# Kernel optimization log

Hardware: AMD Instinct MI355X
Metric: run time of the kernel (lower is better)

The kernel has to match this reference:

```python
import jax, jax.numpy as jnp
import numpy as np

B, S, D = 1, 2048, 2048
H, KVH = 32, 8
HD = D // H          # 64
N_REP = H // KVH     # 4
ROPE_THETA = 10000.0
NEG = -1e9


def setup_inputs() -> dict:
    key = jax.random.key(0)
    ks = jax.random.split(key, 8)
    x = jax.random.normal(ks[0], (B, S, D), dtype=jnp.float32)
    # RoPE tables: freqs_cis[t, j] = exp(i * t * theta^{-2j/HD}), j in [0, HD/2)
    inv_freq = 1.0 / (ROPE_THETA ** (jnp.arange(0, HD, 2, dtype=jnp.float32) / HD))
    angles = jnp.arange(S, dtype=jnp.float32)[:, None] * inv_freq[None, :]  # (S, HD/2)
    freqs_cos = jnp.cos(angles)
    freqs_sin = jnp.sin(angles)
    # causal additive mask (S, S)
    mask = jnp.where(jnp.tril(jnp.ones((S, S), dtype=bool)), 0.0, NEG).astype(jnp.float32)
    sc = 0.02
    wq = jax.random.normal(ks[1], (D, H * HD), dtype=jnp.float32) * sc
    wk = jax.random.normal(ks[2], (D, KVH * HD), dtype=jnp.float32) * sc
    wv = jax.random.normal(ks[3], (D, KVH * HD), dtype=jnp.float32) * sc
    wo = jax.random.normal(ks[4], (H * HD, D), dtype=jnp.float32) * sc
    fw = jax.random.normal(ks[5], (HD, HD), dtype=jnp.float32) * sc
    fb = jnp.zeros((HD,), dtype=jnp.float32)
    return {"x": x, "freqs_cos": freqs_cos, "freqs_sin": freqs_sin, "mask": mask,
            "wq": wq, "wk": wk, "wv": wv, "wo": wo, "fw": fw, "fb": fb,
            "start_pos": 0}


def _rope(t, cos, sin):
    # t: (B, S, h, HD) -> complex rotate pairs along last dim
    tr = t.reshape(*t.shape[:-1], HD // 2, 2)
    c = cos[None, :, None, :]  # (1, S, 1, HD/2)
    s = sin[None, :, None, :]
    re = tr[..., 0] * c - tr[..., 1] * s
    im = tr[..., 0] * s + tr[..., 1] * c
    return jnp.stack([re, im], axis=-1).reshape(t.shape)


def reference(x, freqs_cos, freqs_sin, mask, wq, wk, wv, wo, fw, fb, start_pos):
    b, s, _ = x.shape
    xq = (x @ wq).reshape(b, s, H, HD)
    xk = (x @ wk).reshape(b, s, KVH, HD)
    xv = (x @ wv).reshape(b, s, KVH, HD)
    xq = _rope(xq, freqs_cos, freqs_sin)
    xk = _rope(xk, freqs_cos, freqs_sin)
    # GQA: repeat kv heads (repeat_interleave on head dim)
    keys = jnp.repeat(xk, N_REP, axis=2)    # (b, s, H, HD)
    values = jnp.repeat(xv, N_REP, axis=2)
    q = xq.transpose(0, 2, 1, 3)            # (b, H, s, HD)
    k = keys.transpose(0, 2, 1, 3)
    v = values.transpose(0, 2, 1, 3)
    scores = jnp.einsum("bhqd,bhkd->bhqk", q, k) / np.sqrt(HD).astype(np.float32)
    scores = scores + mask[None, None, :, :]
    probs = jax.nn.softmax(scores.astype(jnp.float32), axis=-1).astype(q.dtype)
    out = jnp.einsum("bhqk,bhkd->bhqd", probs, v)  # (b, H, s, HD)
    # shared per-head FFN: Linear(HD, HD) + SiLU, vectorized over heads
    out = jax.nn.silu(out @ fw + fb)
    out = out.transpose(0, 2, 1, 3).reshape(b, s, H * HD)
    return out @ wo
```

## Files before the change

kernel.cpp:

```cpp
#include <hip/hip_runtime.h>
#include <stdint.h>

#define S_LEN 2048
#define DMODEL 2048
#define NH 32
#define NKV 8
#define HD 64

typedef __attribute__((ext_vector_type(8))) __bf16 bf16x8;
typedef __attribute__((ext_vector_type(4))) float f32x4;
typedef __attribute__((ext_vector_type(16))) float f32x16;

__device__ __forceinline__ unsigned short f2bf(float f) {
    union { float f; uint32_t u; } v; v.f = f;
    uint32_t u = v.u;
    u += 0x7FFFu + ((u >> 16) & 1u);
    return (unsigned short)(u >> 16);
}

__device__ __forceinline__ uint32_t cvt_pk_bf16(float lo, float hi) {
    uint32_t r;
    asm("v_cvt_pk_bf16_f32 %0, %1, %2" : "=v"(r) : "v"(lo), "v"(hi));
    return r;
}

#define GLDS16(g, l)                                                          \
    __builtin_amdgcn_global_load_lds(                                         \
        (const __attribute__((address_space(1))) unsigned int*)(g),           \
        (__attribute__((address_space(3))) unsigned int*)(l), 16, 0, 0)

__device__ const int kUQT[24] = {15,15,7,14,14,13,13,6,12,12,11,11,5,10,10,9,9,4,8,8,3,2,1,0};
__device__ const int kUCH[24] = {0,1,0,0,1,0,1,0,0,1,0,1,0,0,1,0,1,0,0,1,0,0,0,0};
__device__ const int kUSP[24] = {1,1,0,1,1,1,1,0,1,1,1,1,0,1,1,1,1,0,1,1,0,0,0,0};

__global__ void cast_bf16_kernel(const float* __restrict__ src,
                                 unsigned short* __restrict__ dst, int n) {
    int g = (blockIdx.x * blockDim.x + threadIdx.x) * 8;
    if (g >= n) return;
    float4 a = *(const float4*)&src[g];
    float4 b = *(const float4*)&src[g + 4];
    unsigned short o[8];
    o[0] = f2bf(a.x); o[1] = f2bf(a.y); o[2] = f2bf(a.z); o[3] = f2bf(a.w);
    o[4] = f2bf(b.x); o[5] = f2bf(b.y); o[6] = f2bf(b.z); o[7] = f2bf(b.w);
    *(uint4*)&dst[g] = *(const uint4*)o;
}

__global__ void prep_transpose_kernel(
    const float* __restrict__ wq, const float* __restrict__ wk,
    const float* __restrict__ wv, const float* __restrict__ wo,
    const float* __restrict__ fw, unsigned short* __restrict__ wqkvT,
    unsigned short* __restrict__ woT, unsigned short* __restrict__ fwT) {
    __shared__ float tile[32][33];
    const int z = blockIdx.z;
    const float* src;
    unsigned short* dst;
    int R, C;
    if (z == 0)      { src = wq; dst = wqkvT;                         R = 2048; C = 2048; }
    else if (z == 1) { src = wk; dst = wqkvT + (size_t)2048 * 2048;   R = 2048; C = 512;  if (blockIdx.x >= 16) return; }
    else if (z == 2) { src = wv; dst = wqkvT + (size_t)2560 * 2048;   R = 2048; C = 512;  if (blockIdx.x >= 16) return; }
    else if (z == 3) { src = wo; dst = woT;                           R = 2048; C = 2048; }
    else             { src = fw; dst = fwT;                           R = 64;   C = 64;   if (blockIdx.x >= 2 || blockIdx.y >= 2) return; }
    int c0 = blockIdx.x * 32, r0 = blockIdx.y * 32;
    int tx = threadIdx.x, ty = threadIdx.y;
#pragma unroll
    for (int i = 0; i < 32; i += 8)
        tile[ty + i][tx] = src[(size_t)(r0 + ty + i) * C + c0 + tx];
    __syncthreads();
#pragma unroll
    for (int i = 0; i < 32; i += 8)
        dst[(size_t)(c0 + ty + i) * R + r0 + tx] = f2bf(tile[tx][ty + i]);
}

template <int MODE>
__global__ __launch_bounds__(256) void gemm_bt_kernel(
    const unsigned short* __restrict__ A, const unsigned short* __restrict__ BT,
    float* __restrict__ C0, unsigned short* __restrict__ Qb,
    unsigned short* __restrict__ Kb, unsigned short* __restrict__ VT,
    const float* __restrict__ fcos, const float* __restrict__ fsin,
    int M, int N, int K) {
    __shared__ unsigned short As[3][128 * 32];
    __shared__ unsigned short Bs[3][64 * 32];
    const int t = threadIdx.x;
    const int lane = t & 63, wave = t >> 6;
    const int wr = wave >> 1, wc = wave & 1;
    const int gx = gridDim.x;
    const int nwg = gx * gridDim.y;
    const int wg = blockIdx.y * gx + blockIdx.x;
    const int swz = (wg & 7) * (nwg >> 3) + (wg >> 3);
    const int m0 = (swz % gx) * 128, n0 = (swz / gx) * 64;
    const int l15 = lane & 15, lhi = lane >> 4;
    f32x4 acc[4][2] = {};
    const unsigned short* ga = A + (size_t)(m0 + (t >> 2)) * K + (t & 3) * 8;
    const unsigned short* gb = BT + (size_t)(n0 + (t >> 2)) * K + (t & 3) * 8;
    const int nk = K >> 5;

#define GSTAGE(buf, kt)                                                       \
    {                                                                         \
        const int k0_ = (kt) * 32;                                            \
        GLDS16(ga + k0_, &As[buf][t * 8]);                                    \
        GLDS16(ga + (size_t)64 * K + k0_, &As[buf][t * 8 + 64 * 32]);         \
        if (t < 256) GLDS16(gb + k0_, &Bs[buf][t * 8]);                       \
    }

    GSTAGE(0, 0);
    GSTAGE(1, 1);

    int cb = 0, pfb = 2;
#pragma unroll 1
    for (int kt = 0; kt < nk; ++kt) {
        if (kt + 1 < nk) asm volatile("s_waitcnt vmcnt(3)" ::: "memory");
        else             asm volatile("s_waitcnt vmcnt(0)" ::: "memory");
        __builtin_amdgcn_s_barrier();
        __builtin_amdgcn_sched_barrier(0);
        if (kt + 2 < nk) GSTAGE(pfb, kt + 2);
        pfb = (pfb == 2) ? 0 : pfb + 1;
        const int mycb = cb;
        cb = (cb == 2) ? 0 : cb + 1;
        bf16x8 af[4], bfr[2];
#pragma unroll
        for (int m = 0; m < 4; m++)
            af[m] = *(const bf16x8*)&As[mycb][(wr * 64 + m * 16 + l15) * 32 + lhi * 8];
#pragma unroll
        for (int n = 0; n < 2; n++)
            bfr[n] = *(const bf16x8*)&Bs[mycb][(wc * 32 + n * 16 + l15) * 32 + lhi * 8];
#pragma unroll
        for (int m = 0; m < 4; m++)
#pragma unroll
            for (int n = 0; n < 2; n++)
                acc[m][n] = __builtin_amdgcn_mfma_f32_16x16x32_bf16(
                    af[m], bfr[n], acc[m][n], 0, 0, 0);
    }
#undef GSTAGE
    if (MODE == 0) {
#pragma unroll
        for (int m = 0; m < 4; m++) {
            int row = m0 + wr * 64 + m * 16 + lhi * 4;
#pragma unroll
            for (int n = 0; n < 2; n++) {
                int col = n0 + wc * 32 + n * 16 + l15;
#pragma unroll
                for (int r = 0; r < 4; r++)
                    C0[(size_t)(row + r) * N + col] = acc[m][n][r];
            }
        }
    } else {
        const int nblk = n0 >> 6;
        if (nblk < 40) {
            const float CS = 0.125f * 1.44269504f;
            const bool isQ = (nblk < 32);
            unsigned short* dst = isQ ? Qb + (size_t)nblk * (S_LEN * HD)
                                      : Kb + (size_t)(nblk - 32) * (S_LEN * HD);
#pragma unroll
            for (int m = 0; m < 4; m++) {
#pragma unroll
                for (int n = 0; n < 2; n++) {
                    int col = wc * 32 + n * 16 + l15;
                    int i = col >> 1;
                    float sgn = (col & 1) ? 1.f : -1.f;
#pragma unroll
                    for (int r = 0; r < 4; r++) {
                        int s = m0 + wr * 64 + m * 16 + lhi * 4 + r;
                        float c = fcos[s * 32 + i], sn = fsin[s * 32 + i];
                        float v = acc[m][n][r];
                        float pv = __shfl_xor(v, 1);
                        float o = fmaf(pv, sgn * sn, v * c);
                        if (isQ) o *= CS;
                        dst[(size_t)s * HD + col] = f2bf(o);
                    }
                }
            }
        } else {
            const int kvh = nblk - 40;
            unsigned short* ldsT = (unsigned short*)As;
            __syncthreads();
#pragma unroll
            for (int m = 0; m < 4; m++)
#pragma unroll
                for (int n = 0; n < 2; n++) {
                    int d = wc * 32 + n * 16 + l15;
#pragma unroll
                    for (int r = 0; r < 4; r++) {
                        int sl = wr * 64 + m * 16 + lhi * 4 + r;
                        ldsT[d * 130 + sl] = f2bf(acc[m][n][r]);
                    }
                }
            __syncthreads();
            const int d = t >> 2, sc = (t & 3) * 32;
            unsigned short* dst = VT + ((size_t)kvh * HD + d) * S_LEN + m0 + sc;
            const unsigned short* srcl = &ldsT[d * 130 + sc];
#pragma unroll
            for (int j = 0; j < 16; j++)
                ((uint32_t*)dst)[j] = *(const uint32_t*)&srcl[2 * j];
        }
    }
}

__global__ __launch_bounds__(256) void flash_kernel(
    const unsigned short* __restrict__ Q, const unsigned short* __restrict__ Kg,
    const unsigned short* __restrict__ VTg, unsigned short* __restrict__ O,
    float* __restrict__ Opart, float* __restrict__ ML) {
    __shared__ unsigned short Ks[3][4096];
    __shared__ unsigned short Vs[3][4096];
    const int t = threadIdx.x, lane = t & 63, wave = t >> 6;
    const int l31 = lane & 31, hi = lane >> 5;
    const int bid = blockIdx.x;
    const int h = bid & 31, u = bid >> 5;
    const int qt = kUQT[u], ch = kUCH[u], sp = kUSP[u];
    const int kvh = h >> 2;

    const int kt0 = sp ? ch * (qt + 1) : 0;
    const int ktN = sp ? kt0 + qt + 1 : 2 * qt + 2;

    const int srow = t >> 3;
    const int scol = ((t & 7) * 8) ^ ((srow & 7) * 8);
    const unsigned short* gk = Kg + ((size_t)kvh * S_LEN + srow) * HD + scol;
    const unsigned short* gv = VTg + ((size_t)kvh * HD + srow) * S_LEN + scol;

    const int q0 = qt * 128;
    const int qw0 = q0 + wave * 32;
    const int q = qw0 + l31;

    const unsigned short* qp = Q + ((size_t)h * S_LEN + q) * HD + hi * 8;
    bf16x8 qf0 = *(const bf16x8*)(qp);
    bf16x8 qf1 = *(const bf16x8*)(qp + 16);
    bf16x8 qf2 = *(const bf16x8*)(qp + 32);
    bf16x8 qf3 = *(const bf16x8*)(qp + 48);

    f32x16 oacc0 = {}, oacc1 = {};
    float mrun = -1e30f, lrun = 0.f;

    {
        const size_t kva = (size_t)kt0 * 64, kvb = kva + 64;
        GLDS16(gk + kva * HD, &Ks[0][t * 8]);
        GLDS16(gk + (kva + 32) * HD, &Ks[0][t * 8 + 2048]);
        GLDS16(gv + kva, &Vs[0][t * 8]);
        GLDS16(gv + (size_t)32 * S_LEN + kva, &Vs[0][t * 8 + 2048]);
        GLDS16(gk + kvb * HD, &Ks[1][t * 8]);
        GLDS16(gk + (kvb + 32) * HD, &Ks[1][t * 8 + 2048]);
        GLDS16(gv + kvb, &Vs[1][t * 8]);
        GLDS16(gv + (size_t)32 * S_LEN + kvb, &Vs[1][t * 8 + 2048]);
    }

    int cb = 0, pfb = 2;
#pragma unroll 1
    for (int kt = kt0; kt < ktN; ++kt) {
        if (kt + 1 < ktN) asm volatile("s_waitcnt vmcnt(4)" ::: "memory");
        else              asm volatile("s_waitcnt vmcnt(0)" ::: "memory");
        __builtin_amdgcn_s_barrier();
        __builtin_amdgcn_sched_barrier(0);
        if (kt + 2 < ktN) {
            const size_t kvp = (size_t)(kt + 2) * 64;
            GLDS16(gk + kvp * HD, &Ks[pfb][t * 8]);
            GLDS16(gk + (kvp + 32) * HD, &Ks[pfb][t * 8 + 2048]);
            GLDS16(gv + kvp, &Vs[pfb][t * 8]);
            GLDS16(gv + (size_t)32 * S_LEN + kvp, &Vs[pfb][t * 8 + 2048]);
        }
        pfb = (pfb == 2) ? 0 : pfb + 1;
        const int kv0 = kt * 64;
        const int mycb = cb;
        cb = (cb == 2) ? 0 : cb + 1;
        if (kv0 > qw0 + 31) continue;
        const unsigned short* ksb = Ks[mycb];
        const unsigned short* vsb = Vs[mycb];
        const int sw = (l31 & 7) * 8;
        f32x16 s0 = {}, s1 = {};
#pragma unroll
        for (int kc = 0; kc < 4; kc++) {
            bf16x8 k0 = *(const bf16x8*)&ksb[l31 * 64 + ((16 * kc + 8 * hi) ^ sw)];
            bf16x8 k1 = *(const bf16x8*)&ksb[(32 + l31) * 64 + ((16 * kc + 8 * hi) ^ sw)];
            bf16x8 qc = (kc == 0) ? qf0 : (kc == 1) ? qf1 : (kc == 2) ? qf2 : qf3;
            s0 = __builtin_amdgcn_mfma_f32_32x32x16_bf16(k0, qc, s0, 0, 0, 0);
            s1 = __builtin_amdgcn_mfma_f32_32x32x16_bf16(k1, qc, s1, 0, 0, 0);
        }
        float p0[16], p1[16];
        if (kv0 + 63 <= qw0) {
#pragma unroll
            for (int r = 0; r < 16; r++) { p0[r] = s0[r]; p1[r] = s1[r]; }
        } else {
#pragma unroll
            for (int r = 0; r < 16; r++) {
                int rr = (r & 3) + 8 * (r >> 2) + 4 * hi;
                p0[r] = (kv0 + rr <= q) ? s0[r] : -1e30f;
                p1[r] = (kv0 + 32 + rr <= q) ? s1[r] : -1e30f;
            }
        }
        float t8[8];
#pragma unroll
        for (int r = 0; r < 8; r++)
            t8[r] = fmaxf(fmaxf(p0[r], p0[r + 8]), fmaxf(p1[r], p1[r + 8]));
        float lm = fmaxf(fmaxf(fmaxf(t8[0], t8[4]), fmaxf(t8[1], t8[5])),
                         fmaxf(fmaxf(t8[2], t8[6]), fmaxf(t8[3], t8[7])));
        if (!__all(lm - mrun <= 8.f)) {
            float rm = fmaxf(lm, __shfl_xor(lm, 32));
            float mnew = fmaxf(mrun, rm);
            float sc = exp2f(mrun - mnew);
            mrun = mnew;
            lrun *= sc;
            oacc0 *= sc;
            oacc1 *= sc;
        }
#pragma unroll
        for (int r = 0; r < 16; r++) {
            p0[r] = exp2f(p0[r] - mrun);
            p1[r] = exp2f(p1[r] - mrun);
        }
        float sA = 0.f, sB = 0.f, sC = 0.f, sD = 0.f;
#pragma unroll
        for (int r = 0; r < 4; r++) {
            sA += p0[r] + p1[r];
            sB += p0[r + 4] + p1[r + 4];
            sC += p0[r + 8] + p1[r + 8];
            sD += p0[r + 12] + p1[r + 12];
        }
        lrun += (sA + sB) + (sC + sD);
        bf16x8 pf[4];
#pragma unroll
        for (int kc = 0; kc < 4; kc++) {
            const int sub = (kc & 1) * 8;
            uint32_t Wl0, Wl1, Wh0, Wh1;
            if (kc < 2) {
                Wl0 = cvt_pk_bf16(p0[sub + 0], p0[sub + 1]);
                Wl1 = cvt_pk_bf16(p0[sub + 2], p0[sub + 3]);
                Wh0 = cvt_pk_bf16(p0[sub + 4], p0[sub + 5]);
                Wh1 = cvt_pk_bf16(p0[sub + 6], p0[sub + 7]);
            } else {
                Wl0 = cvt_pk_bf16(p1[sub + 0], p1[sub + 1]);
                Wl1 = cvt_pk_bf16(p1[sub + 2], p1[sub + 3]);
                Wh0 = cvt_pk_bf16(p1[sub + 4], p1[sub + 5]);
                Wh1 = cvt_pk_bf16(p1[sub + 6], p1[sub + 7]);
            }
            uint32_t sw0 = hi ? Wl0 : Wh0, sw1 = hi ? Wl1 : Wh1;
            uint32_t rc0 = __shfl_xor((int)sw0, 32);
            uint32_t rc1 = __shfl_xor((int)sw1, 32);
            uint32_t kp0 = hi ? Wh0 : Wl0, kp1 = hi ? Wh1 : Wl1;
            uint32_t F0 = hi ? rc0 : kp0;
            uint32_t F1 = hi ? rc1 : kp1;
            uint32_t F2 = hi ? kp0 : rc0;
            uint32_t F3 = hi ? kp1 : rc1;
            uint4 fu = {F0, F1, F2, F3};
            pf[kc] = *(const bf16x8*)&fu;
        }
#pragma unroll
        for (int kc = 0; kc < 4; kc++) {
            bf16x8 v0 = *(const bf16x8*)&vsb[l31 * 64 + ((16 * kc + 8 * hi) ^ sw)];
            bf16x8 v1 = *(const bf16x8*)&vsb[(32 + l31) * 64 + ((16 * kc + 8 * hi) ^ sw)];
            oacc0 = __builtin_amdgcn_mfma_f32_32x32x16_bf16(v0, pf[kc], oacc0, 0, 0, 0);
            oacc1 = __builtin_amdgcn_mfma_f32_32x32x16_bf16(v1, pf[kc], oacc1, 0, 0, 0);
        }
    }
    lrun += __shfl_xor(lrun, 32);
    const int qrow = wave * 32 + l31;
    if (sp) {
        const int pidx = (h * 8 + (qt - 8)) * 2 + ch;
        float* po = Opart + ((size_t)pidx * 128 + qrow) * 64 + 4 * hi;
#pragma unroll
        for (int g = 0; g < 4; g++) {
            float4 a = {oacc0[4 * g], oacc0[4 * g + 1], oacc0[4 * g + 2], oacc0[4 * g + 3]};
            *(float4*)(po + 8 * g) = a;
            float4 b = {oacc1[4 * g], oacc1[4 * g + 1], oacc1[4 * g + 2], oacc1[4 * g + 3]};
            *(float4*)(po + 32 + 8 * g) = b;
        }
        if (hi == 0) {
            ML[((size_t)pidx * 128 + qrow) * 2] = mrun;
            ML[((size_t)pidx * 128 + qrow) * 2 + 1] = lrun;
        }
    } else {
        float rinv = 1.f / lrun;
        unsigned short* ob = O + ((size_t)h * S_LEN + q) * HD + 4 * hi;
#pragma unroll
        for (int g = 0; g < 4; g++) {
            uint32_t a0 = cvt_pk_bf16(oacc0[4 * g] * rinv, oacc0[4 * g + 1] * rinv);
            uint32_t a1 = cvt_pk_bf16(oacc0[4 * g + 2] * rinv, oacc0[4 * g + 3] * rinv);
            uint2 u0 = {a0, a1};
            *(uint2*)(ob + 8 * g) = u0;
            uint32_t b0 = cvt_pk_bf16(oacc1[4 * g] * rinv, oacc1[4 * g + 1] * rinv);
            uint32_t b1 = cvt_pk_bf16(oacc1[4 * g + 2] * rinv, oacc1[4 * g + 3] * rinv);
            uint2 u1 = {b0, b1};
            *(uint2*)(ob + 32 + 8 * g) = u1;
        }
    }
}

__global__ __launch_bounds__(256) void flash_combine_kernel(
    const float* __restrict__ Opart, const float* __restrict__ ML,
    unsigned short* __restrict__ attn) {
    const int bid = blockIdx.x;
    const int h = bid & 31, j = bid >> 5;
    const int qt = 8 + j;
    const int t = threadIdx.x;
    const int qrow = t >> 1, d0 = (t & 1) * 32;
    const int base = (h * 8 + j) * 2;
    const float mA = ML[((size_t)base * 128 + qrow) * 2];
    const float lA = ML[((size_t)base * 128 + qrow) * 2 + 1];
    const float mB = ML[((size_t)(base + 1) * 128 + qrow) * 2];
    const float lB = ML[((size_t)(base + 1) * 128 + qrow) * 2 + 1];
    const float m = fmaxf(mA, mB);
    const float wA = exp2f(mA - m), wB = exp2f(mB - m);
    const float rinv = 1.f / (lA * wA + lB * wB);
    const float* pA = Opart + ((size_t)base * 128 + qrow) * 64 + d0;
    const float* pB = Opart + ((size_t)(base + 1) * 128 + qrow) * 64 + d0;
    unsigned short* po = attn + ((size_t)h * S_LEN + qt * 128 + qrow) * HD + d0;
#pragma unroll
    for (int dd = 0; dd < 32; dd += 8) {
        float4 a0 = *(const float4*)&pA[dd], a1 = *(const float4*)&pA[dd + 4];
        float4 b0 = *(const float4*)&pB[dd], b1 = *(const float4*)&pB[dd + 4];
        unsigned short o[8];
        o[0] = f2bf((a0.x * wA + b0.x * wB) * rinv);
        o[1] = f2bf((a0.y * wA + b0.y * wB) * rinv);
        o[2] = f2bf((a0.z * wA + b0.z * wB) * rinv);
        o[3] = f2bf((a0.w * wA + b0.w * wB) * rinv);
        o[4] = f2bf((a1.x * wA + b1.x * wB) * rinv);
        o[5] = f2bf((a1.y * wA + b1.y * wB) * rinv);
        o[6] = f2bf((a1.z * wA + b1.z * wB) * rinv);
        o[7] = f2bf((a1.w * wA + b1.w * wB) * rinv);
        *(uint4*)&po[dd] = *(const uint4*)o;
    }
}

__global__ __launch_bounds__(256) void fw_silu_kernel(
    const unsigned short* __restrict__ AT, const unsigned short* __restrict__ fwT,
    const float* __restrict__ fb, unsigned short* __restrict__ h2) {
    const int t = threadIdx.x, lane = t & 63, wave = t >> 6;
    const int l15 = lane & 15, lhi = lane >> 4;
    const int r0 = blockIdx.x * 64 + wave * 16;
    const unsigned short* ap = AT + (size_t)(r0 + l15) * HD + lhi * 8;
    bf16x8 a0 = *(const bf16x8*)ap;
    bf16x8 a1 = *(const bf16x8*)(ap + 32);
    f32x4 acc[4] = {};
#pragma unroll
    for (int nb = 0; nb < 4; nb++) {
        const unsigned short* bp = fwT + (size_t)(nb * 16 + l15) * HD + lhi * 8;
        bf16x8 b0 = *(const bf16x8*)bp;
        bf16x8 b1 = *(const bf16x8*)(bp + 32);
        acc[nb] = __builtin_amdgcn_mfma_f32_16x16x32_bf16(a0, b0, acc[nb], 0, 0, 0);
        acc[nb] = __builtin_amdgcn_mfma_f32_16x16x32_bf16(a1, b1, acc[nb], 0, 0, 0);
    }
#pragma unroll
    for (int nb = 0; nb < 4; nb++) {
        int col = nb * 16 + l15;
        float bias = fb[col];
#pragma unroll
        for (int r = 0; r < 4; r++) {
            int row = r0 + lhi * 4 + r;
            int s = row & (S_LEN - 1), hh = row >> 11;
            float x = acc[nb][r] + bias;
            float sg = 1.f / (1.f + exp2f(-x * 1.44269504f));
            h2[(size_t)s * DMODEL + hh * HD + col] = f2bf(x * sg);
        }
    }
}

extern "C" void kernel_launch(void* const* d_in, const int* in_sizes, int n_in,
                              void* d_out, int out_size, void* d_ws, size_t ws_size,
                              hipStream_t stream) {
    const float* x = (const float*)d_in[0];
    const float* fcos = (const float*)d_in[1];
    const float* fsin = (const float*)d_in[2];
    const float* wq = (const float*)d_in[4];
    const float* wk = (const float*)d_in[5];
    const float* wv = (const float*)d_in[6];
    const float* wo = (const float*)d_in[7];
    const float* fw = (const float*)d_in[8];
    const float* fb = (const float*)d_in[9];
    float* out = (float*)d_out;

    char* ws = (char*)d_ws;
    size_t off = 0;
    auto alloc = [&](size_t bytes) {
        void* p = ws + off;
        off += (bytes + 255) & ~(size_t)255;
        return p;
    };
    unsigned short* wqkvT = (unsigned short*)alloc((size_t)3072 * 2048 * 2);
    unsigned short* woT   = (unsigned short*)alloc((size_t)2048 * 2048 * 2);
    unsigned short* fwT   = (unsigned short*)alloc((size_t)64 * 64 * 2);
    unsigned short* Qb    = (unsigned short*)alloc((size_t)NH * S_LEN * HD * 2);
    unsigned short* Kb    = (unsigned short*)alloc((size_t)NKV * S_LEN * HD * 2);
    unsigned short* VT    = (unsigned short*)alloc((size_t)NKV * HD * S_LEN * 2);
    unsigned short* xb    = (unsigned short*)alloc((size_t)2048 * 2048 * 2);
    float*          ML    = (float*)alloc((size_t)512 * 128 * 2 * 4);
    unsigned short* attn  = (unsigned short*)alloc((size_t)NH * S_LEN * HD * 2);
    float*          Opart = (float*)alloc((size_t)512 * 128 * 64 * 4);
    unsigned short* h2 = xb;

    cast_bf16_kernel<<<2048, 256, 0, stream>>>(x, xb, 2048 * 2048);
    prep_transpose_kernel<<<dim3(64, 64, 5), dim3(32, 8), 0, stream>>>(
        wq, wk, wv, wo, fw, wqkvT, woT, fwT);

    gemm_bt_kernel<1><<<dim3(16, 48), 256, 0, stream>>>(
        xb, wqkvT, nullptr, Qb, Kb, VT, fcos, fsin, 2048, 3072, 2048);

    flash_kernel<<<768, 256, 0, stream>>>(Qb, Kb, VT, attn, Opart, ML);
    flash_combine_kernel<<<256, 256, 0, stream>>>(Opart, ML, attn);

    fw_silu_kernel<<<1024, 256, 0, stream>>>(attn, fwT, fb, h2);

    gemm_bt_kernel<0><<<dim3(16, 32), 256, 0, stream>>>(
        h2, woT, out, nullptr, nullptr, nullptr, nullptr, nullptr,
        2048, 2048, 2048);
}
```

Baseline: 169.7 us.

## Halve flash KV tile to 32 and fuse x cast into prep kernel

The flash attention kernel now streams K/V in 32-row tiles instead of 64. It uses half the LDS per stage, one QK MFMA chain per tile and a new V swizzle, and doubles the iteration count. The causal range bounds and split boundaries are recomputed accordingly. Separately, the fp32-to-bf16 cast of x is merged into the weight transpose prep kernel as an extra grid z-slice, saving one launch. Smaller tiles cut LDS use and register pressure, possibly raising occupancy and giving finer causal skipping, at the cost of more barriers and loop overhead per unit of work.

```diff
diff --git a/kernel.cpp b/kernel.cpp
--- a/kernel.cpp
+++ b/kernel.cpp
@@ -33,35 +33,32 @@
 __device__ const int kUCH[24] = {0,1,0,0,1,0,1,0,0,1,0,1,0,0,1,0,1,0,0,1,0,0,0,0};
 __device__ const int kUSP[24] = {1,1,0,1,1,1,1,0,1,1,1,1,0,1,1,1,1,0,1,1,0,0,0,0};
 
-__global__ void cast_bf16_kernel(const float* __restrict__ src,
-                                 unsigned short* __restrict__ dst, int n) {
-    int g = (blockIdx.x * blockDim.x + threadIdx.x) * 8;
-    if (g >= n) return;
-    float4 a = *(const float4*)&src[g];
-    float4 b = *(const float4*)&src[g + 4];
-    unsigned short o[8];
-    o[0] = f2bf(a.x); o[1] = f2bf(a.y); o[2] = f2bf(a.z); o[3] = f2bf(a.w);
-    o[4] = f2bf(b.x); o[5] = f2bf(b.y); o[6] = f2bf(b.z); o[7] = f2bf(b.w);
-    *(uint4*)&dst[g] = *(const uint4*)o;
-}
-
-__global__ void prep_transpose_kernel(
+__global__ void prep_kernel(
     const float* __restrict__ wq, const float* __restrict__ wk,
     const float* __restrict__ wv, const float* __restrict__ wo,
-    const float* __restrict__ fw, unsigned short* __restrict__ wqkvT,
-    unsigned short* __restrict__ woT, unsigned short* __restrict__ fwT) {
+    const float* __restrict__ fw, const float* __restrict__ x,
+    unsigned short* __restrict__ wqkvT, unsigned short* __restrict__ woT,
+    unsigned short* __restrict__ fwT, unsigned short* __restrict__ xb) {
+    const int z = blockIdx.z;
+    const int tx = threadIdx.x, ty = threadIdx.y;
+    if (z == 5) {
+        int base = (blockIdx.y * 64 + blockIdx.x) * 1024 + (ty * 32 + tx) * 4;
+        float4 a = *(const float4*)&x[base];
+        ushort4 o;
+        o.x = f2bf(a.x); o.y = f2bf(a.y); o.z = f2bf(a.z); o.w = f2bf(a.w);
+        *(ushort4*)&xb[base] = o;
+        return;
+    }
     __shared__ float tile[32][33];
-    const int z = blockIdx.z;
     const float* src;
     unsigned short* dst;
     int R, C;
-    if (z == 0)      { src = wq; dst = wqkvT;                         R = 2048; C = 2048; }
-    else if (z == 1) { src = wk; dst = wqkvT + (size_t)2048 * 2048;   R = 2048; C = 512;  if (blockIdx.x >= 16) return; }
-    else if (z == 2) { src = wv; dst = wqkvT + (size_t)2560 * 2048;   R = 2048; C = 512;  if (blockIdx.x >= 16) return; }
-    else if (z == 3) { src = wo; dst = woT;                           R = 2048; C = 2048; }
-    else             { src = fw; dst = fwT;                           R = 64;   C = 64;   if (blockIdx.x >= 2 || blockIdx.y >= 2) return; }
+    if (z == 0)      { src = wq; dst = wqkvT;                       R = 2048; C = 2048; }
+    else if (z == 1) { src = wk; dst = wqkvT + (size_t)2048 * 2048; R = 2048; C = 512;  if (blockIdx.x >= 16) return; }
+    else if (z == 2) { src = wv; dst = wqkvT + (size_t)2560 * 2048; R = 2048; C = 512;  if (blockIdx.x >= 16) return; }
+    else if (z == 3) { src = wo; dst = woT;                         R = 2048; C = 2048; }
+    else             { src = fw; dst = fwT;                         R = 64;   C = 64;   if (blockIdx.x >= 2 || blockIdx.y >= 2) return; }
     int c0 = blockIdx.x * 32, r0 = blockIdx.y * 32;
-    int tx = threadIdx.x, ty = threadIdx.y;
 #pragma unroll
     for (int i = 0; i < 32; i += 8)
         tile[ty + i][tx] = src[(size_t)(r0 + ty + i) * C + c0 + tx];
@@ -199,8 +196,8 @@
     const unsigned short* __restrict__ Q, const unsigned short* __restrict__ Kg,
     const unsigned short* __restrict__ VTg, unsigned short* __restrict__ O,
     float* __restrict__ Opart, float* __restrict__ ML) {
-    __shared__ unsigned short Ks[3][4096];
-    __shared__ unsigned short Vs[3][4096];
+    __shared__ unsigned short Ks[3][2048];
+    __shared__ unsigned short Vs[3][2048];
     const int t = threadIdx.x, lane = t & 63, wave = t >> 6;
     const int l31 = lane & 31, hi = lane >> 5;
     const int bid = blockIdx.x;
@@ -208,13 +205,15 @@
     const int qt = kUQT[u], ch = kUCH[u], sp = kUSP[u];
     const int kvh = h >> 2;
 
-    const int kt0 = sp ? ch * (qt + 1) : 0;
-    const int ktN = sp ? kt0 + qt + 1 : 2 * qt + 2;
+    const int kt0 = sp ? ch * (2 * qt + 2) : 0;
+    const int ktN = kt0 + (sp ? (2 * qt + 2) : (4 * qt + 4));
 
     const int srow = t >> 3;
     const int scol = ((t & 7) * 8) ^ ((srow & 7) * 8);
     const unsigned short* gk = Kg + ((size_t)kvh * S_LEN + srow) * HD + scol;
-    const unsigned short* gv = VTg + ((size_t)kvh * HD + srow) * S_LEN + scol;
+    const int vrow = t >> 2;
+    const int vcol = (((t & 3) ^ (vrow & 3)) * 8);
+    const unsigned short* gv = VTg + ((size_t)kvh * HD + vrow) * S_LEN + vcol;
 
     const int q0 = qt * 128;
     const int qw0 = q0 + wave * 32;
@@ -229,65 +228,53 @@
     f32x16 oacc0 = {}, oacc1 = {};
     float mrun = -1e30f, lrun = 0.f;
 
-    {
-        const size_t kva = (size_t)kt0 * 64, kvb = kva + 64;
-        GLDS16(gk + kva * HD, &Ks[0][t * 8]);
-        GLDS16(gk + (kva + 32) * HD, &Ks[0][t * 8 + 2048]);
-        GLDS16(gv + kva, &Vs[0][t * 8]);
-        GLDS16(gv + (size_t)32 * S_LEN + kva, &Vs[0][t * 8 + 2048]);
-        GLDS16(gk + kvb * HD, &Ks[1][t * 8]);
-        GLDS16(gk + (kvb + 32) * HD, &Ks[1][t * 8 + 2048]);
-        GLDS16(gv + kvb, &Vs[1][t * 8]);
-        GLDS16(gv + (size_t)32 * S_LEN + kvb, &Vs[1][t * 8 + 2048]);
-    }
+#define FSTAGE(buf, kt)                                                       \
+    {                                                                         \
+        const size_t kv_ = (size_t)(kt) * 32;                                 \
+        GLDS16(gk + kv_ * HD, &Ks[buf][t * 8]);                               \
+        GLDS16(gv + kv_, &Vs[buf][t * 8]);                                    \
+    }
+
+    FSTAGE(0, kt0);
+    FSTAGE(1, kt0 + 1);
 
     int cb = 0, pfb = 2;
 #pragma unroll 1
     for (int kt = kt0; kt < ktN; ++kt) {
-        if (kt + 1 < ktN) asm volatile("s_waitcnt vmcnt(4)" ::: "memory");
+        if (kt + 1 < ktN) asm volatile("s_waitcnt vmcnt(2)" ::: "memory");
         else              asm volatile("s_waitcnt vmcnt(0)" ::: "memory");
         __builtin_amdgcn_s_barrier();
         __builtin_amdgcn_sched_barrier(0);
-        if (kt + 2 < ktN) {
-            const size_t kvp = (size_t)(kt + 2) * 64;
-            GLDS16(gk + kvp * HD, &Ks[pfb][t * 8]);
-            GLDS16(gk + (kvp + 32) * HD, &Ks[pfb][t * 8 + 2048]);
-            GLDS16(gv + kvp, &Vs[pfb][t * 8]);
-            GLDS16(gv + (size_t)32 * S_LEN + kvp, &Vs[pfb][t * 8 + 2048]);
-        }
+        if (kt + 2 < ktN) FSTAGE(pfb, kt + 2);
         pfb = (pfb == 2) ? 0 : pfb + 1;
-        const int kv0 = kt * 64;
+        const int kv0 = kt * 32;
         const int mycb = cb;
         cb = (cb == 2) ? 0 : cb + 1;
         if (kv0 > qw0 + 31) continue;
         const unsigned short* ksb = Ks[mycb];
         const unsigned short* vsb = Vs[mycb];
         const int sw = (l31 & 7) * 8;
-        f32x16 s0 = {}, s1 = {};
+        f32x16 s0 = {};
 #pragma unroll
         for (int kc = 0; kc < 4; kc++) {
             bf16x8 k0 = *(const bf16x8*)&ksb[l31 * 64 + ((16 * kc + 8 * hi) ^ sw)];
-            bf16x8 k1 = *(const bf16x8*)&ksb[(32 + l31) * 64 + ((16 * kc + 8 * hi) ^ sw)];
             bf16x8 qc = (kc == 0) ? qf0 : (kc == 1) ? qf1 : (kc == 2) ? qf2 : qf3;
             s0 = __builtin_amdgcn_mfma_f32_32x32x16_bf16(k0, qc, s0, 0, 0, 0);
-            s1 = __builtin_amdgcn_mfma_f32_32x32x16_bf16(k1, qc, s1, 0, 0, 0);
-        }
-        float p0[16], p1[16];
-        if (kv0 + 63 <= qw0) {
-#pragma unroll
-            for (int r = 0; r < 16; r++) { p0[r] = s0[r]; p1[r] = s1[r]; }
+        }
+        float p0[16];
+        if (kv0 + 31 <= qw0) {
+#pragma unroll
+            for (int r = 0; r < 16; r++) p0[r] = s0[r];
         } else {
 #pragma unroll
             for (int r = 0; r < 16; r++) {
                 int rr = (r & 3) + 8 * (r >> 2) + 4 * hi;
                 p0[r] = (kv0 + rr <= q) ? s0[r] : -1e30f;
-                p1[r] = (kv0 + 32 + rr <= q) ? s1[r] : -1e30f;
             }
         }
         float t8[8];
 #pragma unroll
-        for (int r = 0; r < 8; r++)
-            t8[r] = fmaxf(fmaxf(p0[r], p0[r + 8]), fmaxf(p1[r], p1[r + 8]));
+        for (int r = 0; r < 8; r++) t8[r] = fmaxf(p0[r], p0[r + 8]);
         float lm = fmaxf(fmaxf(fmaxf(t8[0], t8[4]), fmaxf(t8[1], t8[5])),
                          fmaxf(fmaxf(t8[2], t8[6]), fmaxf(t8[3], t8[7])));
         if (!__all(lm - mrun <= 8.f)) {
@@ -300,35 +287,22 @@
             oacc1 *= sc;
         }
 #pragma unroll
-        for (int r = 0; r < 16; r++) {
-            p0[r] = exp2f(p0[r] - mrun);
-            p1[r] = exp2f(p1[r] - mrun);
-        }
-        float sA = 0.f, sB = 0.f, sC = 0.f, sD = 0.f;
+        for (int r = 0; r < 16; r++) p0[r] = exp2f(p0[r] - mrun);
+        float sA = 0.f, sB = 0.f;
 #pragma unroll
         for (int r = 0; r < 4; r++) {
-            sA += p0[r] + p1[r];
-            sB += p0[r + 4] + p1[r + 4];
-            sC += p0[r + 8] + p1[r + 8];
-            sD += p0[r + 12] + p1[r + 12];
-        }
-        lrun += (sA + sB) + (sC + sD);
-        bf16x8 pf[4];
-#pragma unroll
-        for (int kc = 0; kc < 4; kc++) {
-            const int sub = (kc & 1) * 8;
-            uint32_t Wl0, Wl1, Wh0, Wh1;
-            if (kc < 2) {
-                Wl0 = cvt_pk_bf16(p0[sub + 0], p0[sub + 1]);
-                Wl1 = cvt_pk_bf16(p0[sub + 2], p0[sub + 3]);
-                Wh0 = cvt_pk_bf16(p0[sub + 4], p0[sub + 5]);
-                Wh1 = cvt_pk_bf16(p0[sub + 6], p0[sub + 7]);
-            } else {
-                Wl0 = cvt_pk_bf16(p1[sub + 0], p1[sub + 1]);
-                Wl1 = cvt_pk_bf16(p1[sub + 2], p1[sub + 3]);
-                Wh0 = cvt_pk_bf16(p1[sub + 4], p1[sub + 5]);
-                Wh1 = cvt_pk_bf16(p1[sub + 6], p1[sub + 7]);
-            }
+            sA += p0[r] + p0[r + 4];
+            sB += p0[r + 8] + p0[r + 12];
+        }
+        lrun += sA + sB;
+        bf16x8 pf[2];
+#pragma unroll
+        for (int kc = 0; kc < 2; kc++) {
+            const int sub = kc * 8;
+            uint32_t Wl0 = cvt_pk_bf16(p0[sub + 0], p0[sub + 1]);
+            uint32_t Wl1 = cvt_pk_bf16(p0[sub + 2], p0[sub + 3]);
+            uint32_t Wh0 = cvt_pk_bf16(p0[sub + 4], p0[sub + 5]);
+            uint32_t Wh1 = cvt_pk_bf16(p0[sub + 6], p0[sub + 7]);
             uint32_t sw0 = hi ? Wl0 : Wh0, sw1 = hi ? Wl1 : Wh1;
             uint32_t rc0 = __shfl_xor((int)sw0, 32);
             uint32_t rc1 = __shfl_xor((int)sw1, 32);
@@ -341,13 +315,15 @@
             pf[kc] = *(const bf16x8*)&fu;
         }
 #pragma unroll
-        for (int kc = 0; kc < 4; kc++) {
-            bf16x8 v0 = *(const bf16x8*)&vsb[l31 * 64 + ((16 * kc + 8 * hi) ^ sw)];
-            bf16x8 v1 = *(const bf16x8*)&vsb[(32 + l31) * 64 + ((16 * kc + 8 * hi) ^ sw)];
+        for (int kc = 0; kc < 2; kc++) {
+            const int vs0 = ((kc * 2 + hi) ^ (l31 & 3)) * 8;
+            bf16x8 v0 = *(const bf16x8*)&vsb[l31 * 32 + vs0];
+            bf16x8 v1 = *(const bf16x8*)&vsb[(32 + l31) * 32 + vs0];
             oacc0 = __builtin_amdgcn_mfma_f32_32x32x16_bf16(v0, pf[kc], oacc0, 0, 0, 0);
             oacc1 = __builtin_amdgcn_mfma_f32_32x32x16_bf16(v1, pf[kc], oacc1, 0, 0, 0);
         }
     }
+#undef FSTAGE
     lrun += __shfl_xor(lrun, 32);
     const int qrow = wave * 32 + l31;
     if (sp) {
@@ -483,9 +459,8 @@
     float*          Opart = (float*)alloc((size_t)512 * 128 * 64 * 4);
     unsigned short* h2 = xb;
 
-    cast_bf16_kernel<<<2048, 256, 0, stream>>>(x, xb, 2048 * 2048);
-    prep_transpose_kernel<<<dim3(64, 64, 5), dim3(32, 8), 0, stream>>>(
-        wq, wk, wv, wo, fw, wqkvT, woT, fwT);
+    prep_kernel<<<dim3(64, 64, 6), dim3(32, 8), 0, stream>>>(
+        wq, wk, wv, wo, fw, x, wqkvT, woT, fwT, xb);
 
     gemm_bt_kernel<1><<<dim3(16, 48), 256, 0, stream>>>(
         xb, wqkvT, nullptr, Qb, Kb, VT, fcos, fsin, 2048, 3072, 2048);
```

Measured after the change: 159.9 us. 5.8% less time.
